# Optimization experiments

Measured on AMD Instinct MI355X. Metric: run time of the kernel, lower is better.

The kernel has to match this reference:

```python
import jax, jax.numpy as jnp
import numpy as np

EMB = 128
HEADS = 4
OUT = EMB // HEADS
NL = 50000
NR = 50000
E = 800000


def setup_inputs() -> dict:
    key = jax.random.key(0)
    ks = jax.random.split(key, 20)
    s = 0.05  # param init scale
    f32 = jnp.float32
    return {
        "left_features": jax.random.normal(ks[0], (NL, EMB), f32),
        "edge_indices": jax.random.randint(ks[1], (2, E), 0, NL),  # NL == NR
        "edge_features": jax.random.normal(ks[2], (E, EMB), f32),
        "right_features": jax.random.normal(ks[3], (NR, EMB), f32),
        # GATv2Conv params
        "W_l": jax.random.normal(ks[4], (EMB, HEADS * OUT), f32) * s,
        "b_l": jnp.zeros((HEADS * OUT,), f32),
        "W_r": jax.random.normal(ks[5], (EMB, HEADS * OUT), f32) * s,
        "b_r": jnp.zeros((HEADS * OUT,), f32),
        "W_e": jax.random.normal(ks[6], (EMB, HEADS * OUT), f32) * s,
        "att": jax.random.normal(ks[7], (HEADS, OUT), f32) * s,
        "b_conv": jnp.zeros((HEADS * OUT,), f32),
        # LayerNorm
        "ln_g": jnp.ones((EMB,), f32),
        "ln_b": jnp.zeros((EMB,), f32),
        # output MLP
        "W1": jax.random.normal(ks[8], (2 * EMB, EMB), f32) * s,
        "b1": jnp.zeros((EMB,), f32),
        "W2": jax.random.normal(ks[9], (EMB, EMB), f32) * s,
        "b2": jnp.zeros((EMB,), f32),
    }


def reference(left_features, edge_indices, edge_features, right_features,
              W_l, b_l, W_r, b_r, W_e, att, b_conv, ln_g, ln_b,
              W1, b1, W2, b2):
    H, O = att.shape
    n_right = right_features.shape[0]
    src = edge_indices[0]
    dst = edge_indices[1]

    # linear projections (GATv2: separate lin_l for src, lin_r for dst, lin_edge no bias)
    x_l = (left_features @ W_l + b_l).reshape(-1, H, O)   # [NL,H,O]
    x_r = (right_features @ W_r + b_r).reshape(-1, H, O)  # [NR,H,O]
    e = (edge_features @ W_e).reshape(-1, H, O)           # [E,H,O]

    # per-edge GATv2 attention logits
    z = jax.nn.leaky_relu(x_l[src] + x_r[dst] + e, 0.2)   # [E,H,O]
    logits = jnp.einsum('eho,ho->eh', z, att)             # [E,H]

    # segment softmax over destination nodes
    m = jax.ops.segment_max(logits, dst, num_segments=n_right)
    m = jnp.where(jnp.isfinite(m), m, 0.0)  # guard empty segments
    ex = jnp.exp(logits - m[dst])
    den = jax.ops.segment_sum(ex, dst, num_segments=n_right)
    alpha = ex / (den[dst] + 1e-16)                       # [E,H]

    # message = transformed src feature weighted by alpha, scatter-add to dst
    msg = jax.ops.segment_sum(x_l[src] * alpha[:, :, None], dst,
                              num_segments=n_right)       # [NR,H,O]
    msg = msg.reshape(n_right, H * O) + b_conv            # concat heads + bias

    # LayerNorm
    mu = jnp.mean(msg, axis=-1, keepdims=True)
    var = jnp.mean(jnp.square(msg - mu), axis=-1, keepdims=True)
    msg = (msg - mu) * jax.lax.rsqrt(var + 1e-5) * ln_g + ln_b

    # out MLP on [msg, right_features]
    h = jnp.concatenate([msg, right_features], axis=-1)
    h = jax.nn.relu(h @ W1 + b1)
    return h @ W2 + b2
```

## Files before the change

kernel.cpp:

```cpp
#include <hip/hip_runtime.h>
#include <math.h>

#define EMB 128

typedef __bf16 bf16x8 __attribute__((ext_vector_type(8)));
typedef float f32x4 __attribute__((ext_vector_type(4)));


__device__ __forceinline__ int incl_scan_256(int v, int* lds) {
    int tid = threadIdx.x;
    lds[tid] = v;
    __syncthreads();
    #pragma unroll
    for (int off = 1; off < 256; off <<= 1) {
        int t = (tid >= off) ? lds[tid - off] : 0;
        __syncthreads();
        lds[tid] += t;
        __syncthreads();
    }
    return lds[tid];
}

__global__ void pack_all_kernel(
    const float* __restrict__ W_e, const float* __restrict__ W_l,
    const float* __restrict__ W_r, const float* __restrict__ W1,
    const float* __restrict__ W2,
    __bf16* __restrict__ we, __bf16* __restrict__ wl, __bf16* __restrict__ wr,
    __bf16* __restrict__ w1, __bf16* __restrict__ w2)
{
    int idx = blockIdx.x * 256 + threadIdx.x;
    const float* W; __bf16* P; int K; int base;
    if (idx < 2048)       { W = W_e; P = we; K = 128; base = 0; }
    else if (idx < 4096)  { W = W_l; P = wl; K = 128; base = 2048; }
    else if (idx < 6144)  { W = W_r; P = wr; K = 128; base = 4096; }
    else if (idx < 10240) { W = W1;  P = w1; K = 256; base = 6144; }
    else                  { W = W2;  P = w2; K = 128; base = 10240; }
    idx -= base;
    const int ksteps = K >> 5;
    const int l = idx & 63;
    const int s = (idx >> 6) % ksteps;
    const int t = (idx >> 6) / ksteps;
    #pragma unroll
    for (int j = 0; j < 8; ++j) {
        int k = s * 32 + ((l >> 4) * 8) + j;
        int n = t * 16 + (l & 15);
        P[(size_t)idx * 8 + j] = (__bf16)W[(size_t)k * EMB + n];
    }
}

__device__ __forceinline__ void proj4_compute(
    const __bf16* Wl, const float* __restrict__ X, const float* __restrict__ bias,
    float* __restrict__ Y, int M, int relu, int blk, int tid)
{
    const int l = tid & 63, wv = tid >> 6;
    const int q = l >> 4, c = l & 15;
    const int rbase = blk * 64 + wv * 16;

    int arow = rbase + c; if (arow >= M) arow = M - 1;
    const float* Ap = X + (size_t)arow * EMB + q * 8;

    f32x4 acc[8];
    #pragma unroll
    for (int t = 0; t < 8; ++t) acc[t] = (f32x4){0.f, 0.f, 0.f, 0.f};

    #pragma unroll
    for (int s = 0; s < 4; ++s) {
        float4 a0 = *(const float4*)(Ap + s * 32);
        float4 a1 = *(const float4*)(Ap + s * 32 + 4);
        bf16x8 af;
        af[0] = (__bf16)a0.x; af[1] = (__bf16)a0.y; af[2] = (__bf16)a0.z; af[3] = (__bf16)a0.w;
        af[4] = (__bf16)a1.x; af[5] = (__bf16)a1.y; af[6] = (__bf16)a1.z; af[7] = (__bf16)a1.w;
        #pragma unroll
        for (int t = 0; t < 8; ++t) {
            bf16x8 bf = *reinterpret_cast<const bf16x8*>(&Wl[((size_t)(t * 4 + s) * 64 + l) * 8]);
            acc[t] = __builtin_amdgcn_mfma_f32_16x16x32_bf16(af, bf, acc[t], 0, 0, 0);
        }
    }

    const int r0 = rbase + q * 4;
    #pragma unroll
    for (int t = 0; t < 8; ++t) {
        const int col = t * 16 + c;
        const float b = bias ? bias[col] : 0.f;
        #pragma unroll
        for (int i = 0; i < 4; ++i) {
            const int r = r0 + i;
            if (r < M) {
                float v = acc[t][i] + b;
                if (relu) v = fmaxf(v, 0.f);
                Y[(size_t)r * EMB + col] = v;
            }
        }
    }
}

template<int KSTEPS>
__global__ __launch_bounds__(256) void proj_mfma(
    const float* __restrict__ X0, const float* __restrict__ X1,
    const __bf16* __restrict__ wpack, const float* __restrict__ bias,
    float* __restrict__ Y, int M, int relu)
{
    __shared__ __attribute__((aligned(16))) __bf16 Wl[KSTEPS * 8 * 64 * 8];
    const int tid = threadIdx.x;
    #pragma unroll
    for (int i = tid; i < KSTEPS * 512; i += 256)
        ((float4*)Wl)[i] = ((const float4*)wpack)[i];
    __syncthreads();

    const int l = tid & 63, wv = tid >> 6;
    const int q = l >> 4, c = l & 15;
    const int rbase = blockIdx.x * 64 + wv * 16;

    int arow = rbase + c; if (arow >= M) arow = M - 1;
    const float* Ap0 = X0 + (size_t)arow * EMB + q * 8;
    const float* Ap1 = (KSTEPS == 8) ? (X1 + (size_t)arow * EMB + q * 8) : Ap0;

    f32x4 acc[8];
    #pragma unroll
    for (int t = 0; t < 8; ++t) acc[t] = (f32x4){0.f, 0.f, 0.f, 0.f};

    #pragma unroll
    for (int s = 0; s < KSTEPS; ++s) {
        const float* bp = (s < 4) ? Ap0 : Ap1;
        const int ss = (s < 4) ? s : s - 4;
        float4 a0 = *(const float4*)(bp + ss * 32);
        float4 a1 = *(const float4*)(bp + ss * 32 + 4);
        bf16x8 af;
        af[0] = (__bf16)a0.x; af[1] = (__bf16)a0.y; af[2] = (__bf16)a0.z; af[3] = (__bf16)a0.w;
        af[4] = (__bf16)a1.x; af[5] = (__bf16)a1.y; af[6] = (__bf16)a1.z; af[7] = (__bf16)a1.w;
        #pragma unroll
        for (int t = 0; t < 8; ++t) {
            bf16x8 bf = *reinterpret_cast<const bf16x8*>(&Wl[((size_t)(t * KSTEPS + s) * 64 + l) * 8]);
            acc[t] = __builtin_amdgcn_mfma_f32_16x16x32_bf16(af, bf, acc[t], 0, 0, 0);
        }
    }

    const int r0 = rbase + q * 4;
    #pragma unroll
    for (int t = 0; t < 8; ++t) {
        const int col = t * 16 + c;
        const float b = bias ? bias[col] : 0.f;
        #pragma unroll
        for (int i = 0; i < 4; ++i) {
            const int r = r0 + i;
            if (r < M) {
                float v = acc[t][i] + b;
                if (relu) v = fmaxf(v, 0.f);
                Y[(size_t)r * EMB + col] = v;
            }
        }
    }
}

__global__ __launch_bounds__(256) void proj_dual(
    const float* __restrict__ XA, const __bf16* __restrict__ wpA,
    const float* __restrict__ bA, float* __restrict__ YA, int MA, int gA,
    const float* __restrict__ XB, const __bf16* __restrict__ wpB,
    const float* __restrict__ bB, float* __restrict__ YB, int MB)
{
    __shared__ __attribute__((aligned(16))) __bf16 Wl[4 * 8 * 64 * 8];
    const int tid = threadIdx.x;
    const bool second = (blockIdx.x >= gA);
    const __bf16* wp = second ? wpB : wpA;
    #pragma unroll
    for (int i = tid; i < 2048; i += 256)
        ((float4*)Wl)[i] = ((const float4*)wp)[i];
    __syncthreads();
    if (second) proj4_compute(Wl, XB, bB, YB, MB, 0, blockIdx.x - gA, tid);
    else        proj4_compute(Wl, XA, bA, YA, MA, 0, blockIdx.x, tid);
}

__global__ __launch_bounds__(256) void edge_kernel(
    const float* __restrict__ EF, const __bf16* __restrict__ wpack,
    const float* __restrict__ xl, const float* __restrict__ xr,
    const int4* __restrict__ edat, const float* __restrict__ att,
    float* __restrict__ exb, int En)
{
    __shared__ __attribute__((aligned(16))) __bf16 Wl[EMB * EMB];
    const int tid = threadIdx.x;
    {
        float4* d4 = (float4*)Wl;
        const float4* s4 = (const float4*)wpack;
        #pragma unroll
        for (int i = 0; i < 8; ++i) d4[tid + 256 * i] = s4[tid + 256 * i];
    }

    const int l = tid & 63, wv = tid >> 6;
    const int q = l >> 4, c = l & 15;
    const int sbase = blockIdx.x * 64 + wv * 16;

    int aslot = sbase + c; if (aslot >= En) aslot = En - 1;
    const int efrow = edat[aslot].x;
    const float* Ap = EF + (size_t)efrow * EMB + q * 8;

    __syncthreads();

    f32x4 acc[8];
    #pragma unroll
    for (int t = 0; t < 8; ++t) acc[t] = (f32x4){0.f, 0.f, 0.f, 0.f};

    #pragma unroll
    for (int s = 0; s < 4; ++s) {
        float4 a0 = *(const float4*)(Ap + s * 32);
        float4 a1 = *(const float4*)(Ap + s * 32 + 4);
        bf16x8 af;
        af[0] = (__bf16)a0.x; af[1] = (__bf16)a0.y; af[2] = (__bf16)a0.z; af[3] = (__bf16)a0.w;
        af[4] = (__bf16)a1.x; af[5] = (__bf16)a1.y; af[6] = (__bf16)a1.z; af[7] = (__bf16)a1.w;
        #pragma unroll
        for (int t = 0; t < 8; ++t) {
            bf16x8 bf = *reinterpret_cast<const bf16x8*>(&Wl[((size_t)(t * 4 + s) * 64 + l) * 8]);
            acc[t] = __builtin_amdgcn_mfma_f32_16x16x32_bf16(af, bf, acc[t], 0, 0, 0);
        }
    }

    __syncthreads();

    float* Z = (float*)Wl + wv * 2048;
    #pragma unroll
    for (int t = 0; t < 8; ++t) {
        const int col = t * 16 + c;
        #pragma unroll
        for (int i = 0; i < 4; ++i) {
            const int le = q * 4 + i;
            Z[le * 128 + (col ^ ((le & 7) << 2))] = acc[t][i];
        }
    }

    const int e = l >> 2, h = l & 3;
    const int slot = sbase + e;
    const int slotc = (slot < En) ? slot : En - 1;
    const int4 ed = edat[slotc];
    const float* xls = xl + (size_t)ed.y * EMB + h * 32;
    const float* xrs = xr + (size_t)ed.z * EMB + h * 32;
    const float* atp = att + h * 32;

    float p = 0.f;
    #pragma unroll
    for (int j4 = 0; j4 < 8; ++j4) {
        f32x4 z4 = *(const f32x4*)&Z[e * 128 + ((h * 32 + j4 * 4) ^ ((e & 7) << 2))];
        float4 a4 = *(const float4*)(xls + j4 * 4);
        float4 b4 = *(const float4*)(xrs + j4 * 4);
        float4 t4 = *(const float4*)(atp + j4 * 4);
        float z0 = z4[0] + a4.x + b4.x; z0 = (z0 > 0.f) ? z0 : 0.2f * z0; p += z0 * t4.x;
        float z1 = z4[1] + a4.y + b4.y; z1 = (z1 > 0.f) ? z1 : 0.2f * z1; p += z1 * t4.y;
        float z2 = z4[2] + a4.z + b4.z; z2 = (z2 > 0.f) ? z2 : 0.2f * z2; p += z2 * t4.z;
        float z3 = z4[3] + a4.w + b4.w; z3 = (z3 > 0.f) ? z3 : 0.2f * z3; p += z3 * t4.w;
    }
    if (slot < En) exb[(size_t)slot * 4 + h] = expf(p);
}

__global__ void hist_kernel(const int* __restrict__ dst, int* __restrict__ counts, int En) {
    int i = blockIdx.x * 256 + threadIdx.x;
    if (i < En) atomicAdd(&counts[dst[i]], 1);
}

__global__ void scan1_kernel(const int* __restrict__ counts, int* __restrict__ bsum, int N) {
    __shared__ int red[4];
    int i = blockIdx.x * 256 + threadIdx.x;
    int v = (i < N) ? counts[i] : 0;
    #pragma unroll
    for (int m = 1; m < 64; m <<= 1) v += __shfl_xor(v, m);
    if ((threadIdx.x & 63) == 0) red[threadIdx.x >> 6] = v;
    __syncthreads();
    if (threadIdx.x == 0) bsum[blockIdx.x] = red[0] + red[1] + red[2] + red[3];
}

__global__ void scan2_kernel(int* __restrict__ bsum, int* __restrict__ boff, int nb,
                             int* __restrict__ offs, int NRtot, int Etot) {
    __shared__ int lds[256];
    int tid = threadIdx.x;
    int v = (tid < nb) ? bsum[tid] : 0;
    int incl = incl_scan_256(v, lds);
    if (tid < nb) boff[tid] = incl - v;
    if (tid == 0) offs[NRtot] = Etot;
}

__global__ void scan3_kernel(const int* __restrict__ counts, const int* __restrict__ boff,
                             int* __restrict__ offs, int* __restrict__ cursor, int N) {
    __shared__ int lds[256];
    int tid = threadIdx.x;
    int i = blockIdx.x * 256 + tid;
    int v = (i < N) ? counts[i] : 0;
    int incl = incl_scan_256(v, lds);
    int excl = incl - v + boff[blockIdx.x];
    if (i < N) { offs[i] = excl; cursor[i] = excl; }
}

__global__ void scatter_kernel(const int* __restrict__ dst, const int* __restrict__ srcv,
                               int* __restrict__ cursor, int4* __restrict__ edat, int En) {
    int i = blockIdx.x * 256 + threadIdx.x;
    if (i < En) {
        int d = dst[i];
        int p = atomicAdd(&cursor[d], 1);
        edat[p] = make_int4(i, srcv[i], d, 0);
    }
}

__global__ __launch_bounds__(128) void msg_ln_kernel(
    const float* __restrict__ xl, const float* __restrict__ exb,
    const int4* __restrict__ edat, const int* __restrict__ offs,
    const float* __restrict__ bconv,
    const float* __restrict__ ln_g, const float* __restrict__ ln_b,
    float* __restrict__ msg)
{
    const int d = blockIdx.x;
    const int tid = threadIdx.x;
    const int h = tid >> 5;
    const int beg = offs[d], end = offs[d + 1];
    const float bc = bconv[tid], g = ln_g[tid], bb = ln_b[tid];

    float acc = 0.f, den = 0.f;
    int i = beg;
    for (; i + 4 <= end; i += 4) {
        int s0 = edat[i + 0].y, s1 = edat[i + 1].y;
        int s2 = edat[i + 2].y, s3 = edat[i + 3].y;
        float ev0 = exb[(size_t)(i + 0) * 4 + h];
        float ev1 = exb[(size_t)(i + 1) * 4 + h];
        float ev2 = exb[(size_t)(i + 2) * 4 + h];
        float ev3 = exb[(size_t)(i + 3) * 4 + h];
        float x0 = xl[(size_t)s0 * EMB + tid];
        float x1 = xl[(size_t)s1 * EMB + tid];
        float x2 = xl[(size_t)s2 * EMB + tid];
        float x3 = xl[(size_t)s3 * EMB + tid];
        acc += ev0 * x0; den += ev0;
        acc += ev1 * x1; den += ev1;
        acc += ev2 * x2; den += ev2;
        acc += ev3 * x3; den += ev3;
    }
    for (; i < end; ++i) {
        int s = edat[i].y;
        float ev = exb[(size_t)i * 4 + h];
        acc += ev * xl[(size_t)s * EMB + tid];
        den += ev;
    }
    float m = acc / (den + 1e-16f) + bc;

    __shared__ float red[2];
    float s1v = m;
    #pragma unroll
    for (int mk = 1; mk < 64; mk <<= 1) s1v += __shfl_xor(s1v, mk);
    if ((tid & 63) == 0) red[tid >> 6] = s1v;
    __syncthreads();
    float mu = (red[0] + red[1]) * (1.f / EMB);
    __syncthreads();
    float cm = m - mu;
    float s2v = cm * cm;
    #pragma unroll
    for (int mk = 1; mk < 64; mk <<= 1) s2v += __shfl_xor(s2v, mk);
    if ((tid & 63) == 0) red[tid >> 6] = s2v;
    __syncthreads();
    float var = (red[0] + red[1]) * (1.f / EMB);
    float y = cm * (1.f / sqrtf(var + 1e-5f)) * g + bb;
    msg[(size_t)d * EMB + tid] = y;
}

extern "C" void kernel_launch(void* const* d_in, const int* in_sizes, int n_in,
                              void* d_out, int out_size, void* d_ws, size_t ws_size,
                              hipStream_t stream) {
    const float* left  = (const float*)d_in[0];
    const int*   eidx  = (const int*)d_in[1];
    const float* ef    = (const float*)d_in[2];
    const float* right = (const float*)d_in[3];
    const float* W_l   = (const float*)d_in[4];
    const float* b_l   = (const float*)d_in[5];
    const float* W_r   = (const float*)d_in[6];
    const float* b_r   = (const float*)d_in[7];
    const float* W_e   = (const float*)d_in[8];
    const float* att   = (const float*)d_in[9];
    const float* bconv = (const float*)d_in[10];
    const float* ln_g  = (const float*)d_in[11];
    const float* ln_b  = (const float*)d_in[12];
    const float* W1    = (const float*)d_in[13];
    const float* b1    = (const float*)d_in[14];
    const float* W2    = (const float*)d_in[15];
    const float* b2    = (const float*)d_in[16];

    const int NLn = in_sizes[0] / EMB;
    const int En  = in_sizes[1] / 2;
    const int NRn = in_sizes[3] / EMB;
    const int* src  = eidx;
    const int* dstp = eidx + En;

    __bf16* we_pack = (__bf16*)d_ws;
    __bf16* wl_pack = we_pack + 16384;
    __bf16* wr_pack = wl_pack + 16384;
    __bf16* w1_pack = wr_pack + 16384;
    __bf16* w2_pack = w1_pack + 32768;
    float* fws = (float*)d_ws + 49152;
    size_t off = 0;
    float* x_l = fws + off; off += (size_t)NLn * EMB;
    float* x_r = fws + off; off += (size_t)NRn * EMB;
    float* exb = fws + off; off += (size_t)En * 4;
    float* msg = fws + off; off += (size_t)NRn * EMB;
    int4* edat  = (int4*)(fws + off);
    int* counts = (int*)(edat + En);
    int* offs   = counts + NRn;
    int* cursor = offs + NRn + 1;
    int* bsum   = cursor + NRn;
    int* boff   = bsum + 256;

    const int nb = (NRn + 255) / 256;
    const int gP_L = (NLn + 63) / 64;
    const int gP_R = (NRn + 63) / 64;
    const int gE64 = (En + 63) / 64;
    const int gE256 = (En + 255) / 256;

    hipMemsetAsync(counts, 0, (size_t)NRn * sizeof(int), stream);

    pack_all_kernel<<<48, 256, 0, stream>>>(W_e, W_l, W_r, W1, W2,
                                            we_pack, wl_pack, wr_pack, w1_pack, w2_pack);

    proj_dual<<<gP_L + gP_R, 256, 0, stream>>>(left, wl_pack, b_l, x_l, NLn, gP_L,
                                               right, wr_pack, b_r, x_r, NRn);

    hist_kernel<<<gE256, 256, 0, stream>>>(dstp, counts, En);
    scan1_kernel<<<nb, 256, 0, stream>>>(counts, bsum, NRn);
    scan2_kernel<<<1, 256, 0, stream>>>(bsum, boff, nb, offs, NRn, En);
    scan3_kernel<<<nb, 256, 0, stream>>>(counts, boff, offs, cursor, NRn);
    scatter_kernel<<<gE256, 256, 0, stream>>>(dstp, src, cursor, edat, En);

    edge_kernel<<<gE64, 256, 0, stream>>>(ef, we_pack, x_l, x_r, edat, att, exb, En);

    msg_ln_kernel<<<NRn, 128, 0, stream>>>(x_l, exb, edat, offs, bconv, ln_g, ln_b, msg);

    proj_mfma<8><<<gP_R, 256, 0, stream>>>(msg, right, w1_pack, b1, x_r, NRn, 1);
    proj_mfma<4><<<gP_R, 256, 0, stream>>>(x_r, nullptr, w2_pack, b2, (float*)d_out, NRn, 0);
}
```

Before: 953.4 us.

## Process edges in original order and scatter exp results via position map

The edge kernel now walks edges in their original order, so edge-feature rows (the largest input, E×128 floats) are read contiguously instead of being gathered through the sorted permutation. Each edge's sorted position is recorded during the scatter pass, and the exp values are written to that position. The sort now stores a compact source-index array instead of 16-byte int4 records, which shrinks the traffic of the scatter and message kernels. In exchange, the exb writes become scattered and the x_r gathers are no longer grouped by destination.

```diff
diff --git a/kernel.cpp b/kernel.cpp
--- a/kernel.cpp
+++ b/kernel.cpp
@@ -173,7 +173,8 @@
 __global__ __launch_bounds__(256) void edge_kernel(
     const float* __restrict__ EF, const __bf16* __restrict__ wpack,
     const float* __restrict__ xl, const float* __restrict__ xr,
-    const int4* __restrict__ edat, const float* __restrict__ att,
+    const int* __restrict__ src, const int* __restrict__ dst,
+    const int* __restrict__ pos, const float* __restrict__ att,
     float* __restrict__ exb, int En)
 {
     __shared__ __attribute__((aligned(16))) __bf16 Wl[EMB * EMB];
@@ -187,11 +188,15 @@
 
     const int l = tid & 63, wv = tid >> 6;
     const int q = l >> 4, c = l & 15;
-    const int sbase = blockIdx.x * 64 + wv * 16;
-
-    int aslot = sbase + c; if (aslot >= En) aslot = En - 1;
-    const int efrow = edat[aslot].x;
-    const float* Ap = EF + (size_t)efrow * EMB + q * 8;
+    const int ebase = blockIdx.x * 64 + wv * 16;
+
+    const int e = l >> 2, h = l & 3;
+    const int eidx_ep = ebase + e;
+    const int eclamp = (eidx_ep < En) ? eidx_ep : En - 1;
+    const int se = src[eclamp], de = dst[eclamp], pe = pos[eclamp];
+
+    int arow = ebase + c; if (arow >= En) arow = En - 1;
+    const float* Ap = EF + (size_t)arow * EMB + q * 8;
 
     __syncthreads();
 
@@ -226,12 +231,8 @@
         }
     }
 
-    const int e = l >> 2, h = l & 3;
-    const int slot = sbase + e;
-    const int slotc = (slot < En) ? slot : En - 1;
-    const int4 ed = edat[slotc];
-    const float* xls = xl + (size_t)ed.y * EMB + h * 32;
-    const float* xrs = xr + (size_t)ed.z * EMB + h * 32;
+    const float* xls = xl + (size_t)se * EMB + h * 32;
+    const float* xrs = xr + (size_t)de * EMB + h * 32;
     const float* atp = att + h * 32;
 
     float p = 0.f;
@@ -246,7 +247,7 @@
         float z2 = z4[2] + a4.z + b4.z; z2 = (z2 > 0.f) ? z2 : 0.2f * z2; p += z2 * t4.z;
         float z3 = z4[3] + a4.w + b4.w; z3 = (z3 > 0.f) ? z3 : 0.2f * z3; p += z3 * t4.w;
     }
-    if (slot < En) exb[(size_t)slot * 4 + h] = expf(p);
+    if (eidx_ep < En) exb[(size_t)pe * 4 + h] = expf(p);
 }
 
 __global__ void hist_kernel(const int* __restrict__ dst, int* __restrict__ counts, int En) {
@@ -287,18 +288,19 @@
 }
 
 __global__ void scatter_kernel(const int* __restrict__ dst, const int* __restrict__ srcv,
-                               int* __restrict__ cursor, int4* __restrict__ edat, int En) {
+                               int* __restrict__ cursor, int* __restrict__ pos,
+                               int* __restrict__ src_sorted, int En) {
     int i = blockIdx.x * 256 + threadIdx.x;
     if (i < En) {
-        int d = dst[i];
-        int p = atomicAdd(&cursor[d], 1);
-        edat[p] = make_int4(i, srcv[i], d, 0);
+        int p = atomicAdd(&cursor[dst[i]], 1);
+        pos[i] = p;
+        src_sorted[p] = srcv[i];
     }
 }
 
 __global__ __launch_bounds__(128) void msg_ln_kernel(
     const float* __restrict__ xl, const float* __restrict__ exb,
-    const int4* __restrict__ edat, const int* __restrict__ offs,
+    const int* __restrict__ src_sorted, const int* __restrict__ offs,
     const float* __restrict__ bconv,
     const float* __restrict__ ln_g, const float* __restrict__ ln_b,
     float* __restrict__ msg)
@@ -312,8 +314,8 @@
     float acc = 0.f, den = 0.f;
     int i = beg;
     for (; i + 4 <= end; i += 4) {
-        int s0 = edat[i + 0].y, s1 = edat[i + 1].y;
-        int s2 = edat[i + 2].y, s3 = edat[i + 3].y;
+        int s0 = src_sorted[i + 0], s1 = src_sorted[i + 1];
+        int s2 = src_sorted[i + 2], s3 = src_sorted[i + 3];
         float ev0 = exb[(size_t)(i + 0) * 4 + h];
         float ev1 = exb[(size_t)(i + 1) * 4 + h];
         float ev2 = exb[(size_t)(i + 2) * 4 + h];
@@ -328,7 +330,7 @@
         acc += ev3 * x3; den += ev3;
     }
     for (; i < end; ++i) {
-        int s = edat[i].y;
+        int s = src_sorted[i];
         float ev = exb[(size_t)i * 4 + h];
         acc += ev * xl[(size_t)s * EMB + tid];
         den += ev;
@@ -392,12 +394,13 @@
     float* x_r = fws + off; off += (size_t)NRn * EMB;
     float* exb = fws + off; off += (size_t)En * 4;
     float* msg = fws + off; off += (size_t)NRn * EMB;
-    int4* edat  = (int4*)(fws + off);
-    int* counts = (int*)(edat + En);
-    int* offs   = counts + NRn;
-    int* cursor = offs + NRn + 1;
-    int* bsum   = cursor + NRn;
-    int* boff   = bsum + 256;
+    int* counts     = (int*)(fws + off);
+    int* offs       = counts + NRn;
+    int* cursor     = offs + NRn + 1;
+    int* bsum       = cursor + NRn;
+    int* boff       = bsum + 256;
+    int* pos        = boff + 256;
+    int* src_sorted = pos + En;
 
     const int nb = (NRn + 255) / 256;
     const int gP_L = (NLn + 63) / 64;
@@ -417,11 +420,11 @@
     scan1_kernel<<<nb, 256, 0, stream>>>(counts, bsum, NRn);
     scan2_kernel<<<1, 256, 0, stream>>>(bsum, boff, nb, offs, NRn, En);
     scan3_kernel<<<nb, 256, 0, stream>>>(counts, boff, offs, cursor, NRn);
-    scatter_kernel<<<gE256, 256, 0, stream>>>(dstp, src, cursor, edat, En);
-
-    edge_kernel<<<gE64, 256, 0, stream>>>(ef, we_pack, x_l, x_r, edat, att, exb, En);
-
-    msg_ln_kernel<<<NRn, 128, 0, stream>>>(x_l, exb, edat, offs, bconv, ln_g, ln_b, msg);
+    scatter_kernel<<<gE256, 256, 0, stream>>>(dstp, src, cursor, pos, src_sorted, En);
+
+    edge_kernel<<<gE64, 256, 0, stream>>>(ef, we_pack, x_l, x_r, src, dstp, pos, att, exb, En);
+
+    msg_ln_kernel<<<NRn, 128, 0, stream>>>(x_l, exb, src_sorted, offs, bconv, ln_g, ln_b, msg);
 
     proj_mfma<8><<<gP_R, 256, 0, stream>>>(msg, right, w1_pack, b1, x_r, NRn, 1);
     proj_mfma<4><<<gP_R, 256, 0, stream>>>(x_r, nullptr, w2_pack, b2, (float*)d_out, NRn, 0);
```

Result: slower. 996.1 us (+4.5%).
